# Optimization experiments

Measured on AMD Instinct MI355X. Metric: run time of the kernel, lower is better.

The kernel has to match this reference:

```python
import jax, jax.numpy as jnp
import numpy as np

N, I, O, G = 16384, 128, 128, 16


def setup_inputs() -> dict:
    key = jax.random.key(0)
    k1, k2, k3 = jax.random.split(key, 3)
    coef_norm = np.sqrt(I) * np.sqrt(G)  # smooth_initialization=False
    return {
        "x": jax.random.normal(k1, (N, I), dtype=jnp.float32),
        "cos_amplitudes": jax.random.normal(k2, (O, I, G), dtype=jnp.float32) / coef_norm,
        "sin_amplitudes": jax.random.normal(k3, (O, I, G), dtype=jnp.float32) / coef_norm,
        "bias": jnp.zeros((O,), dtype=jnp.float32),
        "ln_gamma": jnp.ones((O,), dtype=jnp.float32),
        "ln_beta": jnp.zeros((O,), dtype=jnp.float32),
    }


def reference(x, cos_amplitudes, sin_amplitudes, bias, ln_gamma, ln_beta):
    g = cos_amplitudes.shape[-1]
    # frequencies buffer: init_freq_scale=1.0 -> [1, 2, ..., grid_size]
    freqs = jnp.arange(1, g + 1, dtype=x.dtype)  # (G,)
    phases = x[:, :, None] * freqs               # (N, I, G)
    # contraction expressed as a GEMM instead of broadcast-sum over (N,O,I,G)
    out = jnp.einsum("nig,oig->no", jnp.cos(phases), cos_amplitudes)
    out = out + jnp.einsum("nig,oig->no", jnp.sin(phases), sin_amplitudes)
    out = out + bias  # (N, O)
    # LayerNorm over output_dim, eps=1e-5 (torch default)
    mu = jnp.mean(out, axis=-1, keepdims=True)
    var = jnp.var(out, axis=-1, keepdims=True)
    out = (out - mu) / jnp.sqrt(var + 1e-5) * ln_gamma + ln_beta
    return out
```

## Files before the change

kernel.cpp:

```cpp
#include <hip/hip_runtime.h>
#include <hip/hip_bf16.h>
#include <math.h>

#define N_TOK 16384
#define I_DIM 128
#define O_DIM 128
#define G_DIM 16
#define BN 64
#define CI 4
#define KC (CI * G_DIM * 2)
#define NCHUNK (I_DIM / CI)
#define A_STRIDE 136
#define ABUF (BN * A_STRIDE)
#define C_STRIDE 132

typedef __bf16 bf16x8 __attribute__((ext_vector_type(8)));
typedef float  f32x4  __attribute__((ext_vector_type(4)));

__global__ __launch_bounds__(256) void fkan_pack_b(
    const float* __restrict__ cosA, const float* __restrict__ sinA,
    __bf16* __restrict__ Bp)
{
    int tid = blockIdx.x * 256 + threadIdx.x;
    int gq  = tid & 3;
    int i   = (tid >> 2) & 127;
    int o   = tid >> 9;
    int c   = i >> 2, ks = i & 3;
    int cg  = o >> 5, ot = (o >> 4) & 1, row16 = o & 15;
    int lane = gq * 16 + row16;
    size_t sbase = ((size_t)o * I_DIM + i) * G_DIM + gq * 4;
    float4 cv = *(const float4*)(cosA + sbase);
    float4 sv = *(const float4*)(sinA + sbase);
    bf16x8 v;
    v[0] = (__bf16)cv.x; v[1] = (__bf16)sv.x;
    v[2] = (__bf16)cv.y; v[3] = (__bf16)sv.y;
    v[4] = (__bf16)cv.z; v[5] = (__bf16)sv.z;
    v[6] = (__bf16)cv.w; v[7] = (__bf16)sv.w;
    size_t frag = (((size_t)c * 4 + cg) * 4 + ks) * 2 + ot;
    *(bf16x8*)(Bp + (frag * 64 + lane) * 8) = v;
}

__global__ __launch_bounds__(512) void fkan_main(
    const float* __restrict__ x,
    const __bf16* __restrict__ Bp,
    const float* __restrict__ bias,
    const float* __restrict__ gamma,
    const float* __restrict__ beta,
    float* __restrict__ out)
{
    __shared__ __align__(16) __bf16 smem[2 * ABUF];
    __bf16* A0 = smem;
    __bf16* A1 = smem + ABUF;

    const int t     = threadIdx.x;
    const int lane  = t & 63;
    const int wave  = t >> 6;
    const int rg    = wave >> 2;
    const int cg    = wave & 3;
    const int row16 = lane & 15;
    const int quad  = lane >> 4;
    const int n0    = blockIdx.x * BN;

    const int srow  = (t & 255) >> 2;
    const int sil   = t & 3;
    const int shalf = t >> 8;

    f32x4 acc[2][2];
#pragma unroll
    for (int mt = 0; mt < 2; ++mt)
#pragma unroll
        for (int ot = 0; ot < 2; ++ot)
            acc[mt][ot] = (f32x4){0.f, 0.f, 0.f, 0.f};

    bf16x8 bA[2][4], bB[2][4];

    auto ld_x = [&](int c) -> float {
        return x[(size_t)(n0 + srow) * I_DIM + c * CI + sil];
    };

    auto ld_b = [&](int c, bf16x8 (&b)[2][4]) {
        const bf16x8* base = (const bf16x8*)Bp + ((size_t)(c * 4 + cg) * 8) * 64 + lane;
#pragma unroll
        for (int ks = 0; ks < 4; ++ks)
#pragma unroll
            for (int ot = 0; ot < 2; ++ot)
                b[ot][ks] = base[(ks * 2 + ot) * 64];
    };

    auto stage_a = [&](float xv, __bf16* Ab) {
        float s1, c1;
        __sincosf(xv, &s1, &c1);
        float cb = c1, sb = s1;
        if (shalf) {
            float cd = c1, sd = s1;
#pragma unroll
            for (int d = 0; d < 3; ++d) {
                float cn = cd * cd - sd * sd;
                float sn = 2.f * cd * sd;
                cd = cn; sd = sn;
            }
            cb = cd * c1 - sd * s1;
            sb = sd * c1 + cd * s1;
        }
        __align__(16) __bf16 feat[16];
        float cc_ = cb, ss_ = sb;
#pragma unroll
        for (int j = 0; j < 8; ++j) {
            feat[2 * j]     = (__bf16)cc_;
            feat[2 * j + 1] = (__bf16)ss_;
            float cn = cc_ * c1 - ss_ * s1;
            float sn = ss_ * c1 + cc_ * s1;
            cc_ = cn; ss_ = sn;
        }
        bf16x8* dst = (bf16x8*)(Ab + srow * A_STRIDE + sil * 32 + shalf * 16);
        dst[0] = ((const bf16x8*)feat)[0];
        dst[1] = ((const bf16x8*)feat)[1];
    };

    auto phase = [&](int c, const __bf16* Ar, __bf16* Aw,
                     bf16x8 (&bcur)[2][4], bf16x8 (&bnext)[2][4], float xs, float& xn) {
        const bool pf = (c + 1 < NCHUNK);
        if (pf) ld_b(c + 1, bnext);
        if (c + 2 < NCHUNK) xn = ld_x(c + 2);
        if (pf) stage_a(xs, Aw);

        __builtin_amdgcn_s_setprio(1);
#pragma unroll
        for (int ks = 0; ks < 4; ++ks) {
            bf16x8 a0 = *(const bf16x8*)(Ar + (rg * 32 + row16) * A_STRIDE + ks * 32 + quad * 8);
            bf16x8 a1 = *(const bf16x8*)(Ar + (rg * 32 + 16 + row16) * A_STRIDE + ks * 32 + quad * 8);
            acc[0][0] = __builtin_amdgcn_mfma_f32_16x16x32_bf16(a0, bcur[0][ks], acc[0][0], 0, 0, 0);
            acc[0][1] = __builtin_amdgcn_mfma_f32_16x16x32_bf16(a0, bcur[1][ks], acc[0][1], 0, 0, 0);
            acc[1][0] = __builtin_amdgcn_mfma_f32_16x16x32_bf16(a1, bcur[0][ks], acc[1][0], 0, 0, 0);
            acc[1][1] = __builtin_amdgcn_mfma_f32_16x16x32_bf16(a1, bcur[1][ks], acc[1][1], 0, 0, 0);
        }
        __builtin_amdgcn_s_setprio(0);

        asm volatile("s_waitcnt lgkmcnt(0)" ::: "memory");
        __builtin_amdgcn_sched_barrier(0);
        __builtin_amdgcn_s_barrier();
    };

    float xA = ld_x(0);
    float xB;
    ld_b(0, bA);
    stage_a(xA, A0);
    xB = ld_x(1);
    asm volatile("s_waitcnt lgkmcnt(0)" ::: "memory");
    __builtin_amdgcn_s_barrier();

    for (int cc = 0; cc < NCHUNK / 2; ++cc) {
        phase(2 * cc,     A0, A1, bA, bB, xB, xA);
        phase(2 * cc + 1, A1, A0, bB, bA, xA, xB);
    }

    float* Cs = (float*)smem;
#pragma unroll
    for (int mt = 0; mt < 2; ++mt)
#pragma unroll
        for (int ot = 0; ot < 2; ++ot)
#pragma unroll
            for (int r = 0; r < 4; ++r)
                Cs[(rg * 32 + mt * 16 + quad * 4 + r) * C_STRIDE
                   + cg * 32 + ot * 16 + row16] = acc[mt][ot][r];
    __syncthreads();

    {
        const int r  = t >> 3;
        const int oc = t & 7;
        const float* crow = Cs + r * C_STRIDE + oc * 16;
        float vals[16];
        float sum = 0.f, sumsq = 0.f;
#pragma unroll
        for (int j4 = 0; j4 < 4; ++j4) {
            f32x4 v4 = *(const f32x4*)(crow + 4 * j4);
#pragma unroll
            for (int e = 0; e < 4; ++e) {
                float v = v4[e] + bias[oc * 16 + 4 * j4 + e];
                vals[4 * j4 + e] = v;
                sum += v;
                sumsq += v * v;
            }
        }
        sum   += __shfl_xor(sum, 1);   sum   += __shfl_xor(sum, 2);   sum   += __shfl_xor(sum, 4);
        sumsq += __shfl_xor(sumsq, 1); sumsq += __shfl_xor(sumsq, 2); sumsq += __shfl_xor(sumsq, 4);
        float mu   = sum * (1.0f / O_DIM);
        float var  = sumsq * (1.0f / O_DIM) - mu * mu;
        float rstd = rsqrtf(var + 1e-5f);

        float* orow = out + (size_t)(n0 + r) * O_DIM + oc * 16;
#pragma unroll
        for (int j4 = 0; j4 < 4; ++j4) {
            float4 o4;
            o4.x = (vals[4*j4+0] - mu) * rstd * gamma[oc*16 + 4*j4+0] + beta[oc*16 + 4*j4+0];
            o4.y = (vals[4*j4+1] - mu) * rstd * gamma[oc*16 + 4*j4+1] + beta[oc*16 + 4*j4+1];
            o4.z = (vals[4*j4+2] - mu) * rstd * gamma[oc*16 + 4*j4+2] + beta[oc*16 + 4*j4+2];
            o4.w = (vals[4*j4+3] - mu) * rstd * gamma[oc*16 + 4*j4+3] + beta[oc*16 + 4*j4+3];
            *(float4*)(orow + 4 * j4) = o4;
        }
    }
}

extern "C" void kernel_launch(void* const* d_in, const int* in_sizes, int n_in,
                              void* d_out, int out_size, void* d_ws, size_t ws_size,
                              hipStream_t stream) {
    const float* x     = (const float*)d_in[0];
    const float* cosA  = (const float*)d_in[1];
    const float* sinA  = (const float*)d_in[2];
    const float* bias  = (const float*)d_in[3];
    const float* gamma = (const float*)d_in[4];
    const float* beta  = (const float*)d_in[5];
    float* out = (float*)d_out;

    __bf16* Bp = (__bf16*)d_ws;

    fkan_pack_b<<<dim3((NCHUNK * O_DIM * KC) / 8 / 256), dim3(256), 0, stream>>>(cosA, sinA, Bp);
    fkan_main<<<dim3(N_TOK / BN), dim3(512), 0, stream>>>(x, Bp, bias, gamma, beta, out);
}
```

Baseline: 105.3 us.

## Halve the token tile to 32 rows with 256-thread blocks and coalesce B packing

```diff
diff --git a/kernel.cpp b/kernel.cpp
--- a/kernel.cpp
+++ b/kernel.cpp
@@ -6,7 +6,7 @@
 #define I_DIM 128
 #define O_DIM 128
 #define G_DIM 16
-#define BN 64
+#define BN 32
 #define CI 4
 #define KC (CI * G_DIM * 2)
 #define NCHUNK (I_DIM / CI)
@@ -21,14 +21,14 @@
     const float* __restrict__ cosA, const float* __restrict__ sinA,
     __bf16* __restrict__ Bp)
 {
-    int tid = blockIdx.x * 256 + threadIdx.x;
-    int gq  = tid & 3;
-    int i   = (tid >> 2) & 127;
-    int o   = tid >> 9;
-    int c   = i >> 2, ks = i & 3;
-    int cg  = o >> 5, ot = (o >> 4) & 1, row16 = o & 15;
-    int lane = gq * 16 + row16;
-    size_t sbase = ((size_t)o * I_DIM + i) * G_DIM + gq * 4;
+    int tid   = blockIdx.x * 256 + threadIdx.x;
+    int lane  = tid & 63;
+    int frag  = tid >> 6;
+    int row16 = lane & 15, quad = lane >> 4;
+    int ot = frag & 1, ks = (frag >> 1) & 3, cg = (frag >> 3) & 3, c = frag >> 5;
+    int o  = cg * 32 + ot * 16 + row16;
+    int i  = c * CI + ks;
+    size_t sbase = ((size_t)o * I_DIM + i) * G_DIM + quad * 4;
     float4 cv = *(const float4*)(cosA + sbase);
     float4 sv = *(const float4*)(sinA + sbase);
     bf16x8 v;
@@ -36,11 +36,10 @@
     v[2] = (__bf16)cv.y; v[3] = (__bf16)sv.y;
     v[4] = (__bf16)cv.z; v[5] = (__bf16)sv.z;
     v[6] = (__bf16)cv.w; v[7] = (__bf16)sv.w;
-    size_t frag = (((size_t)c * 4 + cg) * 4 + ks) * 2 + ot;
-    *(bf16x8*)(Bp + (frag * 64 + lane) * 8) = v;
+    *(bf16x8*)(Bp + (size_t)tid * 8) = v;
 }
 
-__global__ __launch_bounds__(512) void fkan_main(
+__global__ __launch_bounds__(256, 2) void fkan_main(
     const float* __restrict__ x,
     const __bf16* __restrict__ Bp,
     const float* __restrict__ bias,
@@ -54,16 +53,14 @@
 
     const int t     = threadIdx.x;
     const int lane  = t & 63;
-    const int wave  = t >> 6;
-    const int rg    = wave >> 2;
-    const int cg    = wave & 3;
+    const int cg    = t >> 6;
     const int row16 = lane & 15;
     const int quad  = lane >> 4;
     const int n0    = blockIdx.x * BN;
 
-    const int srow  = (t & 255) >> 2;
+    const int srow  = (t & 127) >> 2;
     const int sil   = t & 3;
-    const int shalf = t >> 8;
+    const int shalf = t >> 7;
 
     f32x4 acc[2][2];
 #pragma unroll
@@ -127,8 +124,8 @@
         __builtin_amdgcn_s_setprio(1);
 #pragma unroll
         for (int ks = 0; ks < 4; ++ks) {
-            bf16x8 a0 = *(const bf16x8*)(Ar + (rg * 32 + row16) * A_STRIDE + ks * 32 + quad * 8);
-            bf16x8 a1 = *(const bf16x8*)(Ar + (rg * 32 + 16 + row16) * A_STRIDE + ks * 32 + quad * 8);
+            bf16x8 a0 = *(const bf16x8*)(Ar + (row16)      * A_STRIDE + ks * 32 + quad * 8);
+            bf16x8 a1 = *(const bf16x8*)(Ar + (16 + row16) * A_STRIDE + ks * 32 + quad * 8);
             acc[0][0] = __builtin_amdgcn_mfma_f32_16x16x32_bf16(a0, bcur[0][ks], acc[0][0], 0, 0, 0);
             acc[0][1] = __builtin_amdgcn_mfma_f32_16x16x32_bf16(a0, bcur[1][ks], acc[0][1], 0, 0, 0);
             acc[1][0] = __builtin_amdgcn_mfma_f32_16x16x32_bf16(a1, bcur[0][ks], acc[1][0], 0, 0, 0);
@@ -161,7 +158,7 @@
         for (int ot = 0; ot < 2; ++ot)
 #pragma unroll
             for (int r = 0; r < 4; ++r)
-                Cs[(rg * 32 + mt * 16 + quad * 4 + r) * C_STRIDE
+                Cs[(mt * 16 + quad * 4 + r) * C_STRIDE
                    + cg * 32 + ot * 16 + row16] = acc[mt][ot][r];
     __syncthreads();
 
@@ -214,6 +211,6 @@
 
     __bf16* Bp = (__bf16*)d_ws;
 
-    fkan_pack_b<<<dim3((NCHUNK * O_DIM * KC) / 8 / 256), dim3(256), 0, stream>>>(cosA, sinA, Bp);
-    fkan_main<<<dim3(N_TOK / BN), dim3(512), 0, stream>>>(x, Bp, bias, gamma, beta, out);
+    fkan_pack_b<<<dim3(256), dim3(256), 0, stream>>>(cosA, sinA, Bp);
+    fkan_main<<<dim3(N_TOK / BN), dim3(256), 0, stream>>>(x, Bp, bias, gamma, beta, out);
 }
```

After: 98.23 us. -6.7%, faster.
